# Kernel optimization log

Hardware: AMD Instinct MI355X
Metric: run time of the kernel (lower is better)

## Reference

```python
import itertools
import jax, jax.numpy as jnp
import numpy as np


def _interpn_linear(vol, loc):
    """Trilinear sampling with edge-clamping (voxelmorph interpn, fill_value=None).
    vol: [D, H, W, C] float; loc: [D, H, W, 3] float absolute sample coordinates (ij indexing).
    """
    spatial = vol.shape[:-1]
    ndims = len(spatial)
    maxs = jnp.asarray([s - 1 for s in spatial], dtype=loc.dtype)
    cloc = jnp.clip(loc, 0.0, maxs)             # clamp = nearest-neighbor fill outside domain
    loc0 = jnp.floor(cloc)
    loc1 = jnp.minimum(loc0 + 1.0, maxs)
    d1 = loc1 - cloc                            # weight for the low corner (loc0)
    d0 = 1.0 - d1                               # weight for the high corner (loc1)
    loc0i = loc0.astype(jnp.int32)
    loc1i = loc1.astype(jnp.int32)

    # flatten volume and build per-dim strides for linear indexing
    volf = vol.reshape(-1, vol.shape[-1])       # [D*H*W, C]
    strides = np.ones(ndims, dtype=np.int32)
    for d in range(ndims - 2, -1, -1):
        strides[d] = strides[d + 1] * spatial[d + 1]

    out = jnp.zeros(spatial + (vol.shape[-1],), dtype=vol.dtype)
    for corner in itertools.product((0, 1), repeat=ndims):
        idx = jnp.zeros(spatial, dtype=jnp.int32)
        w = jnp.ones(spatial, dtype=vol.dtype)
        for d in range(ndims):
            idx = idx + (loc1i if corner[d] else loc0i)[..., d] * strides[d]
            w = w * (d0 if corner[d] else d1)[..., d]
        out = out + w[..., None] * jnp.take(volf, idx, axis=0)
    return out


def _warp_single(vol, disp):
    """Apply dense displacement field: sample vol at identity grid + disp."""
    spatial = vol.shape[:-1]
    grid = jnp.stack(
        jnp.meshgrid(*[jnp.arange(s, dtype=disp.dtype) for s in spatial], indexing='ij'),
        axis=-1)                                # [D, H, W, 3]
    return _interpn_linear(vol, grid + disp)


def setup_inputs() -> dict:
    key = jax.random.key(0)
    k1, k2 = jax.random.split(key)
    vol = jax.random.normal(k1, (2, 128, 192, 192, 1), dtype=jnp.float32)
    trf = jax.random.normal(k2, (2, 128, 192, 192, 3), dtype=jnp.float32)
    return {"vol": vol, "trf": trf}


def reference(vol, trf):
    # batched dense-warp spatial transformer (single_transform=False)
    return jax.vmap(_warp_single)(vol, trf)
```

## Files before the change

### kernel.cpp

```cpp
#include <hip/hip_runtime.h>
#include <stdint.h>


#define BD 128
#define BH 192
#define BW 192
#define DHW (BD*BH*BW)
#define NB 2

#define TX 16
#define TY 8
#define TZ 8
#define NTX (BW/TX)
#define NTY (BH/TY)
#define NTZ (BD/TZ)
#define NBLK (NTX*NTY*NTZ*NB)
#define NXCD 8

#define SXW 36
#define SYW 16
#define SZW 16
#define SLAB (SXW*SYW)
#define LDSF (SLAB*SZW)
#define NCHUNK (LDSF/4)

typedef float f4v __attribute__((ext_vector_type(4)));

__global__ __launch_bounds__(256, 4) void st_warp_kernel(
    const float* __restrict__ vol,
    const float* __restrict__ trf,
    float* __restrict__ out)
{
    __shared__ __align__(16) float lds[LDSF];

    const int bid = blockIdx.x;
    const int swz = (bid % NXCD) * (NBLK / NXCD) + bid / NXCD;
    int tmp = swz;
    const int txi = tmp % NTX; tmp /= NTX;
    const int tyi = tmp % NTY; tmp /= NTY;
    const int tzi = tmp % NTZ; tmp /= NTZ;
    const int b   = tmp;
    const int tx = txi*TX, ty = tyi*TY, tz = tzi*TZ;

    const int sx = min(max(tx - 8, 0), BW - SXW);
    const int sy = min(max(ty - 4, 0), BH - SYW);
    const int sz = min(max(tz - 4, 0), BD - SZW);

    const int tid = (int)threadIdx.x;
    const float* volb = vol + (size_t)b * DHW;

#pragma unroll
    for (int it = 0; it < 9; ++it) {
        const int f = tid + it*256;
        const int r = f / 9;
        const int c = f - r*9;
        const int zi = r >> 4;
        const int yi = r & 15;
        const float* g = volb + ((size_t)((sz+zi)*BH + (sy+yi)))*BW + sx + c*4;
        __builtin_amdgcn_global_load_lds(
            (const __attribute__((address_space(1))) void*)g,
            (__attribute__((address_space(3))) void*)&lds[f*4],
            16, 0, 0);
    }

    const int xq = tid & 3;
    const int yb = (tid >> 2) & 7;
    const int zb = tid >> 5;
    const int Y  = ty + yb;
    const int Z  = tz + zb;
    const int Xb = tx + xq*4;
    const f4v* trf4 = (const f4v*)trf;
    const size_t rowf4 = ((size_t)((b*BD + Z)*BH + Y)*BW + tx) * 3 / 4;
    const f4v tA = trf4[rowf4 + 3*xq + 0];
    const f4v tB = trf4[rowf4 + 3*xq + 1];
    const f4v tC = trf4[rowf4 + 3*xq + 2];

    __syncthreads();

    const float dzs[4] = {tA.x, tA.w, tB.z, tC.y};
    const float dys[4] = {tA.y, tB.x, tB.w, tC.z};
    const float dxs[4] = {tA.z, tB.y, tC.x, tC.w};
    float res[4];
#pragma unroll
    for (int jj = 0; jj < 4; ++jj) {
        float cz = fminf(fmaxf((float)Z + dzs[jj], 0.f), (float)(BD-1));
        float cy = fminf(fmaxf((float)Y + dys[jj], 0.f), (float)(BH-1));
        float cx = fminf(fmaxf((float)(Xb+jj) + dxs[jj], 0.f), (float)(BW-1));
        float fz = floorf(cz), fy = floorf(cy), fx = floorf(cx);
        int z0 = (int)fz, y0 = (int)fy, x0 = (int)fx;
        int z1 = min(z0+1, BD-1);
        int y1 = min(y0+1, BH-1);
        int x1 = min(x0+1, BW-1);
        float wz = cz - fz, wy = cy - fy, wx = cx - fx;
        float v000,v001,v010,v011,v100,v101,v110,v111;
        bool inwin = (x0 >= sx) & (x1 <= sx+SXW-1) & (y0 >= sy) & (y1 <= sy+SYW-1)
                   & (z0 >= sz) & (z1 <= sz+SZW-1);
        if (inwin) {
            const int xi  = x0 - sx;
            const int xiA = min(xi, SXW-2);
            const bool lo = xi < SXW-1;
            const int rA = (z0 - sz)*SLAB + (y0 - sy)*SXW + xiA;
            const int rB = (z0 - sz)*SLAB + (y1 - sy)*SXW + xiA;
            const int rC = (z1 - sz)*SLAB + (y0 - sy)*SXW + xiA;
            const int rD = (z1 - sz)*SLAB + (y1 - sy)*SXW + xiA;
            float a00 = lds[rA], b00 = lds[rA+1];
            float a01 = lds[rB], b01 = lds[rB+1];
            float a10 = lds[rC], b10 = lds[rC+1];
            float a11 = lds[rD], b11 = lds[rD+1];
            v000 = lo ? a00 : b00;  v001 = b00;
            v010 = lo ? a01 : b01;  v011 = b01;
            v100 = lo ? a10 : b10;  v101 = b10;
            v110 = lo ? a11 : b11;  v111 = b11;
        } else {
            const float* p00 = volb + ((size_t)z0*BH + y0)*BW;
            const float* p01 = volb + ((size_t)z0*BH + y1)*BW;
            const float* p10 = volb + ((size_t)z1*BH + y0)*BW;
            const float* p11 = volb + ((size_t)z1*BH + y1)*BW;
            v000 = p00[x0]; v001 = p00[x1];
            v010 = p01[x0]; v011 = p01[x1];
            v100 = p10[x0]; v101 = p10[x1];
            v110 = p11[x0]; v111 = p11[x1];
        }
        float c00 = v000 + wx*(v001-v000);
        float c01 = v010 + wx*(v011-v010);
        float c10 = v100 + wx*(v101-v100);
        float c11 = v110 + wx*(v111-v110);
        float c0  = c00 + wy*(c01-c00);
        float c1  = c10 + wy*(c11-c10);
        res[jj]   = c0 + wz*(c1-c0);
    }
    f4v r = {res[0], res[1], res[2], res[3]};
    const size_t of4 = ((size_t)((b*BD + Z)*BH + Y)*BW + Xb) / 4;
    __builtin_nontemporal_store(r, &((f4v*)out)[of4]);
}

extern "C" void kernel_launch(void* const* d_in, const int* in_sizes, int n_in,
                              void* d_out, int out_size, void* d_ws, size_t ws_size,
                              hipStream_t stream) {
    const float* vol = (const float*)d_in[0];
    const float* trf = (const float*)d_in[1];
    float* out = (float*)d_out;

    st_warp_kernel<<<dim3(NBLK), dim3(256), 0, stream>>>(vol, trf, out);
}
```

Before: 47.49 us.

## Stream z-slabs through an LDS ring buffer with prefetch across z-steps

Each block now walks four 8-deep z-steps instead of handling one, keeping a 24-slab ring buffer in LDS. Only the new 8 slabs are staged per step while the current step computes, and the next step's displacement values are prefetched into registers. This removes the redundant halo reloads that overlapping per-block windows caused, and overlaps global loads with compute. In exchange the window is narrower in x (32 instead of 36), occupancy drops (launch bounds 3, larger LDS), there are fewer blocks, and more syncs. Ring-slot reuse correctness depends on the async LDS loads finishing before the barrier.

```diff
diff --git a/kernel.cpp b/kernel.cpp
--- a/kernel.cpp
+++ b/kernel.cpp
@@ -10,23 +10,26 @@
 
 #define TX 16
 #define TY 8
-#define TZ 8
 #define NTX (BW/TX)
 #define NTY (BH/TY)
-#define NTZ (BD/TZ)
-#define NBLK (NTX*NTY*NTZ*NB)
+#define NZB 4
+#define NSTEPB 4
+#define NBLK (NTX*NTY*NZB*NB)
 #define NXCD 8
 
-#define SXW 36
+#define SXW 32
 #define SYW 16
-#define SZW 16
 #define SLAB (SXW*SYW)
-#define LDSF (SLAB*SZW)
-#define NCHUNK (LDSF/4)
+#define RING 24
+#define LDSF (RING*SLAB)
 
 typedef float f4v __attribute__((ext_vector_type(4)));
 
-__global__ __launch_bounds__(256, 4) void st_warp_kernel(
+__device__ __forceinline__ int mod24(int z) {
+    return (int)((unsigned)z % 24u);
+}
+
+__global__ __launch_bounds__(256, 3) void st_warp_kernel(
     const float* __restrict__ vol,
     const float* __restrict__ trf,
     float* __restrict__ out)
@@ -35,103 +38,143 @@
 
     const int bid = blockIdx.x;
     const int swz = (bid % NXCD) * (NBLK / NXCD) + bid / NXCD;
-    int tmp = swz;
-    const int txi = tmp % NTX; tmp /= NTX;
-    const int tyi = tmp % NTY; tmp /= NTY;
-    const int tzi = tmp % NTZ; tmp /= NTZ;
-    const int b   = tmp;
-    const int tx = txi*TX, ty = tyi*TY, tz = tzi*TZ;
+    int t = swz;
+    const int txi = t % NTX; t /= NTX;
+    const int tyi = t % NTY; t /= NTY;
+    const int kzb = t % NZB; t /= NZB;
+    const int b   = t;
+    const int tx = txi*TX, ty = tyi*TY;
+    const int zA = kzb * (NSTEPB*8);
 
     const int sx = min(max(tx - 8, 0), BW - SXW);
     const int sy = min(max(ty - 4, 0), BH - SYW);
-    const int sz = min(max(tz - 4, 0), BD - SZW);
 
     const int tid = (int)threadIdx.x;
     const float* volb = vol + (size_t)b * DHW;
-
-#pragma unroll
-    for (int it = 0; it < 9; ++it) {
-        const int f = tid + it*256;
-        const int r = f / 9;
-        const int c = f - r*9;
-        const int zi = r >> 4;
-        const int yi = r & 15;
-        const float* g = volb + ((size_t)((sz+zi)*BH + (sy+yi)))*BW + sx + c*4;
-        __builtin_amdgcn_global_load_lds(
-            (const __attribute__((address_space(1))) void*)g,
-            (__attribute__((address_space(3))) void*)&lds[f*4],
-            16, 0, 0);
-    }
 
     const int xq = tid & 3;
     const int yb = (tid >> 2) & 7;
     const int zb = tid >> 5;
     const int Y  = ty + yb;
-    const int Z  = tz + zb;
     const int Xb = tx + xq*4;
     const f4v* trf4 = (const f4v*)trf;
-    const size_t rowf4 = ((size_t)((b*BD + Z)*BH + Y)*BW + tx) * 3 / 4;
-    const f4v tA = trf4[rowf4 + 3*xq + 0];
-    const f4v tB = trf4[rowf4 + 3*xq + 1];
-    const f4v tC = trf4[rowf4 + 3*xq + 2];
 
+    auto stage = [&](int zfirst, int nslab) {
+        const int nch = nslab << 7;
+        for (int it = 0; it*256 < nch; ++it) {
+            const int f = tid + it*256;
+            if (f < nch) {
+                const int z  = zfirst + (f >> 7);
+                const int s  = f & 127;
+                const int yi = s >> 3;
+                const int c  = s & 7;
+                const int slot = mod24(z);
+                const float* g = volb + ((size_t)(z*BH + sy + yi))*BW + sx + (c<<2);
+                __builtin_amdgcn_global_load_lds(
+                    (const __attribute__((address_space(1))) void*)g,
+                    (__attribute__((address_space(3))) void*)&lds[(slot<<9) + (s<<2)],
+                    16, 0, 0);
+            }
+        }
+    };
+
+    auto load_trf = [&](int ZS, f4v& TA, f4v& TB, f4v& TC) {
+        const size_t rowf4 = ((size_t)((b*BD + ZS + zb)*BH + Y)*BW + tx) * 3 / 4;
+        TA = trf4[rowf4 + 3*xq + 0];
+        TB = trf4[rowf4 + 3*xq + 1];
+        TC = trf4[rowf4 + 3*xq + 2];
+    };
+
+    auto compute = [&](int ZS, f4v tA, f4v tB, f4v tC) {
+        const int Z   = ZS + zb;
+        const int wlo = max(0, ZS - 4);
+        const int whi = min(BD - 1, ZS + 11);
+        const float dzs[4] = {tA.x, tA.w, tB.z, tC.y};
+        const float dys[4] = {tA.y, tB.x, tB.w, tC.z};
+        const float dxs[4] = {tA.z, tB.y, tC.x, tC.w};
+        float res[4];
+#pragma unroll
+        for (int jj = 0; jj < 4; ++jj) {
+            float cz = fminf(fmaxf((float)Z + dzs[jj], 0.f), (float)(BD-1));
+            float cy = fminf(fmaxf((float)Y + dys[jj], 0.f), (float)(BH-1));
+            float cx = fminf(fmaxf((float)(Xb+jj) + dxs[jj], 0.f), (float)(BW-1));
+            float fz = floorf(cz), fy = floorf(cy), fx = floorf(cx);
+            int z0 = (int)fz, y0 = (int)fy, x0 = (int)fx;
+            int z1 = min(z0+1, BD-1);
+            int y1 = min(y0+1, BH-1);
+            int x1 = min(x0+1, BW-1);
+            float wz = cz - fz, wy = cy - fy, wx = cx - fx;
+            float v000,v001,v010,v011,v100,v101,v110,v111;
+            bool inwin = (x0 >= sx) & (x1 <= sx+SXW-1) & (y0 >= sy) & (y1 <= sy+SYW-1)
+                       & (z0 >= wlo) & (z1 <= whi);
+            if (inwin) {
+                const int xi  = x0 - sx;
+                const int xiA = min(xi, SXW-2);
+                const bool lo = xi < SXW-1;
+                int sl0 = mod24(z0);
+                int sl1 = sl0 + 1;
+                sl1 = (sl1 == RING) ? 0 : sl1;
+                sl1 = (z1 == z0) ? sl0 : sl1;
+                const int yt0 = (y0 - sy) << 5, yt1 = (y1 - sy) << 5;
+                const int rA = (sl0<<9) + yt0 + xiA;
+                const int rB = (sl0<<9) + yt1 + xiA;
+                const int rC = (sl1<<9) + yt0 + xiA;
+                const int rD = (sl1<<9) + yt1 + xiA;
+                float a00 = lds[rA], b00 = lds[rA+1];
+                float a01 = lds[rB], b01 = lds[rB+1];
+                float a10 = lds[rC], b10 = lds[rC+1];
+                float a11 = lds[rD], b11 = lds[rD+1];
+                v000 = lo ? a00 : b00;  v001 = b00;
+                v010 = lo ? a01 : b01;  v011 = b01;
+                v100 = lo ? a10 : b10;  v101 = b10;
+                v110 = lo ? a11 : b11;  v111 = b11;
+            } else {
+                const float* p00 = volb + ((size_t)z0*BH + y0)*BW;
+                const float* p01 = volb + ((size_t)z0*BH + y1)*BW;
+                const float* p10 = volb + ((size_t)z1*BH + y0)*BW;
+                const float* p11 = volb + ((size_t)z1*BH + y1)*BW;
+                v000 = p00[x0]; v001 = p00[x1];
+                v010 = p01[x0]; v011 = p01[x1];
+                v100 = p10[x0]; v101 = p10[x1];
+                v110 = p11[x0]; v111 = p11[x1];
+            }
+            float c00 = v000 + wx*(v001-v000);
+            float c01 = v010 + wx*(v011-v010);
+            float c10 = v100 + wx*(v101-v100);
+            float c11 = v110 + wx*(v111-v110);
+            float c0  = c00 + wy*(c01-c00);
+            float c1  = c10 + wy*(c11-c10);
+            res[jj]   = c0 + wz*(c1-c0);
+        }
+        f4v r = {res[0], res[1], res[2], res[3]};
+        const size_t of4 = ((size_t)((b*BD + Z)*BH + Y)*BW + Xb) / 4;
+        __builtin_nontemporal_store(r, &((f4v*)out)[of4]);
+    };
+
+    f4v A0,B0,C0, A1,B1,C1;
+    stage(max(0, zA - 4), (zA == 0) ? 12 : 16);
+    load_trf(zA, A0, B0, C0);
     __syncthreads();
 
-    const float dzs[4] = {tA.x, tA.w, tB.z, tC.y};
-    const float dys[4] = {tA.y, tB.x, tB.w, tC.z};
-    const float dxs[4] = {tA.z, tB.y, tC.x, tC.w};
-    float res[4];
 #pragma unroll
-    for (int jj = 0; jj < 4; ++jj) {
-        float cz = fminf(fmaxf((float)Z + dzs[jj], 0.f), (float)(BD-1));
-        float cy = fminf(fmaxf((float)Y + dys[jj], 0.f), (float)(BH-1));
-        float cx = fminf(fmaxf((float)(Xb+jj) + dxs[jj], 0.f), (float)(BW-1));
-        float fz = floorf(cz), fy = floorf(cy), fx = floorf(cx);
-        int z0 = (int)fz, y0 = (int)fy, x0 = (int)fx;
-        int z1 = min(z0+1, BD-1);
-        int y1 = min(y0+1, BH-1);
-        int x1 = min(x0+1, BW-1);
-        float wz = cz - fz, wy = cy - fy, wx = cx - fx;
-        float v000,v001,v010,v011,v100,v101,v110,v111;
-        bool inwin = (x0 >= sx) & (x1 <= sx+SXW-1) & (y0 >= sy) & (y1 <= sy+SYW-1)
-                   & (z0 >= sz) & (z1 <= sz+SZW-1);
-        if (inwin) {
-            const int xi  = x0 - sx;
-            const int xiA = min(xi, SXW-2);
-            const bool lo = xi < SXW-1;
-            const int rA = (z0 - sz)*SLAB + (y0 - sy)*SXW + xiA;
-            const int rB = (z0 - sz)*SLAB + (y1 - sy)*SXW + xiA;
-            const int rC = (z1 - sz)*SLAB + (y0 - sy)*SXW + xiA;
-            const int rD = (z1 - sz)*SLAB + (y1 - sy)*SXW + xiA;
-            float a00 = lds[rA], b00 = lds[rA+1];
-            float a01 = lds[rB], b01 = lds[rB+1];
-            float a10 = lds[rC], b10 = lds[rC+1];
-            float a11 = lds[rD], b11 = lds[rD+1];
-            v000 = lo ? a00 : b00;  v001 = b00;
-            v010 = lo ? a01 : b01;  v011 = b01;
-            v100 = lo ? a10 : b10;  v101 = b10;
-            v110 = lo ? a11 : b11;  v111 = b11;
-        } else {
-            const float* p00 = volb + ((size_t)z0*BH + y0)*BW;
-            const float* p01 = volb + ((size_t)z0*BH + y1)*BW;
-            const float* p10 = volb + ((size_t)z1*BH + y0)*BW;
-            const float* p11 = volb + ((size_t)z1*BH + y1)*BW;
-            v000 = p00[x0]; v001 = p00[x1];
-            v010 = p01[x0]; v011 = p01[x1];
-            v100 = p10[x0]; v101 = p10[x1];
-            v110 = p11[x0]; v111 = p11[x1];
+    for (int kk = 0; kk < NSTEPB; kk += 2) {
+        {
+            const int zc = zA + kk*8;
+            const int zn = zc + 12;
+            if (zn < BD) stage(zn, min(8, BD - zn));
+            load_trf(zc + 8, A1, B1, C1);
+            compute(zc, A0, B0, C0);
+            __syncthreads();
         }
-        float c00 = v000 + wx*(v001-v000);
-        float c01 = v010 + wx*(v011-v010);
-        float c10 = v100 + wx*(v101-v100);
-        float c11 = v110 + wx*(v111-v110);
-        float c0  = c00 + wy*(c01-c00);
-        float c1  = c10 + wy*(c11-c10);
-        res[jj]   = c0 + wz*(c1-c0);
+        {
+            const int zc = zA + kk*8 + 8;
+            const int zn = zc + 12;
+            if (kk + 2 < NSTEPB && zn < BD) stage(zn, min(8, BD - zn));
+            if (kk + 2 < NSTEPB) load_trf(zc + 8, A0, B0, C0);
+            compute(zc, A1, B1, C1);
+            __syncthreads();
+        }
     }
-    f4v r = {res[0], res[1], res[2], res[3]};
-    const size_t of4 = ((size_t)((b*BD + Z)*BH + Y)*BW + Xb) / 4;
-    __builtin_nontemporal_store(r, &((f4v*)out)[of4]);
 }
 
 extern "C" void kernel_launch(void* const* d_in, const int* in_sizes, int n_in,
```

New measurement: 42.62 us, median of 2. 10.3% less time.
